# Optimization experiments

Hardware: AMD Instinct MI355X
Metric: run time of the kernel (lower is better)

The kernel has to match this reference:

```python
import jax, jax.numpy as jnp
import numpy as np

B, H, S, D = 2, 16, 2048, 64

def setup_inputs() -> dict:
    key = jax.random.key(0)
    kq, kk, kv = jax.random.split(key, 3)
    q = jax.random.normal(kq, (B, H, S, D), dtype=jnp.float32)
    k = jax.random.normal(kk, (B, H, S, D), dtype=jnp.float32)
    v = jax.random.normal(kv, (B, H, S, D), dtype=jnp.float32)
    mask = jnp.tril(jnp.ones((S, S), dtype=bool))  # causal, broadcast over B,H
    return {"q": q, "k": k, "v": v, "mask": mask}

def reference(q, k, v, mask):
    d_k = q.shape[-1]
    # [..., num_q, num_kv]
    qk = jnp.einsum('bhqd,bhkd->bhqk', q, k) / jnp.sqrt(jnp.asarray(d_k, q.dtype))
    qk = jnp.where(mask, qk, -jnp.inf)
    attn = jax.nn.softmax(qk, axis=-1)
    return jnp.einsum('bhqk,bhkd->bhqd', attn, v)
```

## Files before the change

### kernel.cpp

```cpp
#include <hip/hip_runtime.h>

#define SS 2048
#define DD 64
#define BH 32
#define QSCALE 0.1803368801f
#define NCHUNK 40
#define NSLOT (BH * NCHUNK)
#define BUFS 8448

typedef __attribute__((ext_vector_type(8))) short short8;
typedef __attribute__((ext_vector_type(4))) float floatx4;

__device__ __forceinline__ short f2bf(float x) {
  union { float f; unsigned u; } un; un.f = x;
  unsigned r = (un.u + 0x7FFFu + ((un.u >> 16) & 1u)) >> 16;
  return (short)r;
}
__device__ __forceinline__ short f2bf_fast(float x) {
  union { float f; unsigned u; } un; un.f = x;
  return (short)((un.u + 0x8000u) >> 16);
}
__device__ __forceinline__ float fexp2(float x) {
  return __builtin_amdgcn_exp2f(x);
}
__device__ __forceinline__ void gload16(const short* g, short* l) {
  __builtin_amdgcn_global_load_lds(
      (const __attribute__((address_space(1))) void*)g,
      (__attribute__((address_space(3))) void*)l, 16, 0, 0);
}
#define MFMA __builtin_amdgcn_mfma_f32_16x16x32_bf16

__global__ __launch_bounds__(256) void prep_k(const float* __restrict__ K,
                                              short* __restrict__ Kbf) {
  const size_t i = ((size_t)blockIdx.x * 256 + threadIdx.x) * 8;
  floatx4 a = *(const floatx4*)(K + i);
  floatx4 b = *(const floatx4*)(K + i + 4);
  short8 s;
  s[0]=f2bf(a[0]); s[1]=f2bf(a[1]); s[2]=f2bf(a[2]); s[3]=f2bf(a[3]);
  s[4]=f2bf(b[0]); s[5]=f2bf(b[1]); s[6]=f2bf(b[2]); s[7]=f2bf(b[3]);
  *(short8*)(Kbf + i) = s;
}

__device__ __forceinline__ int kperm(int c) {
  return (((c >> 2) & 1) << 4) + ((c >> 3) << 2) + (c & 3);
}

__global__ __launch_bounds__(256) void prep_vtp(const float* __restrict__ V,
                                                short* __restrict__ Vtp) {
  __shared__ short Ts[64][72];
  const int bh = blockIdx.y;
  const int s0 = blockIdx.x * 64;
  const int t = threadIdx.x;
  {
    const int r = t >> 2, c = (t & 3) * 16;
    const float* g = V + ((size_t)bh * SS + s0 + r) * DD + c;
    floatx4 a = *(const floatx4*)g;
    floatx4 b = *(const floatx4*)(g + 4);
    floatx4 cc = *(const floatx4*)(g + 8);
    floatx4 d = *(const floatx4*)(g + 12);
    short8 x0, x1;
    x0[0]=f2bf(a[0]); x0[1]=f2bf(a[1]); x0[2]=f2bf(a[2]); x0[3]=f2bf(a[3]);
    x0[4]=f2bf(b[0]); x0[5]=f2bf(b[1]); x0[6]=f2bf(b[2]); x0[7]=f2bf(b[3]);
    x1[0]=f2bf(cc[0]);x1[1]=f2bf(cc[1]);x1[2]=f2bf(cc[2]);x1[3]=f2bf(cc[3]);
    x1[4]=f2bf(d[0]); x1[5]=f2bf(d[1]); x1[6]=f2bf(d[2]); x1[7]=f2bf(d[3]);
    *(short8*)&Ts[r][c] = x0;
    *(short8*)&Ts[r][c + 8] = x1;
  }
  __syncthreads();
  {
    const int d = t >> 2, cblk = (t & 3) * 16;
    short8 y0, y1;
    #pragma unroll
    for (int j = 0; j < 8; ++j) {
      const int c0 = cblk + j, c1 = cblk + 8 + j;
      y0[j] = Ts[(c0 & 32) + kperm(c0 & 31)][d];
      y1[j] = Ts[(c1 & 32) + kperm(c1 & 31)][d];
    }
    const int kt  = (s0 + cblk) >> 5;
    const int kin = cblk & 31;
    short* o = Vtp + (((size_t)bh * 64 + kt) * 64 + d) * 32 + kin;
    *(short8*)o = y0;
    *(short8*)(o + 8) = y1;
  }
}

__device__ __forceinline__ void y2qc(int y, int& qt, int& c) {
  if (y < 4)       { qt = y;                            c = 0; }
  else if (y < 12) { int i = y - 4;  qt = 4 + (i >> 1); c = i & 1; }
  else if (y < 24) { int i = y - 12; qt = 8 + i / 3;    c = i - (qt - 8) * 3; }
  else             { int i = y - 24; qt = 12 + (i >> 2); c = i & 3; }
}

__global__ __launch_bounds__(256, 4) void sdpa_part(
    const float* __restrict__ Q, const short* __restrict__ Kbf,
    const short* __restrict__ Vtp, float* __restrict__ PO,
    float* __restrict__ PRS) {
  __shared__ __align__(16) short Sh[2][BUFS];

  const int tid  = threadIdx.x;
  const int w    = tid >> 6;
  const int lane = tid & 63;
  const int quad = lane >> 4;
  const int l16  = lane & 15;

  const int bh = blockIdx.x;
  const int y  = 39 - (int)blockIdx.y;
  int qt, c; y2qc(y, qt, c);
  const int kt0 = c * 16;
  const int kt1 = min(kt0 + 16, 4 * qt + 4);
  const int ktd = 4 * qt + w;
  const int qA  = qt * 128 + w * 32;
  const int qB  = qA + 16;

  const size_t base = (size_t)bh * SS * DD;
  const short* kbase = Kbf + base;
  const short* vtb   = Vtp + (size_t)bh * 64 * 2048;

  {
    const short* gk = kbase + (size_t)kt0 * 2048 + w * 512 + lane * 8;
    gload16(gk,        &Sh[0][w * 544]);
    gload16(gk + 2048, &Sh[0][2176 + w * 544]);
    const short* gv = vtb + (size_t)kt0 * 2048 + w * 512 + lane * 8;
    gload16(gv,        &Sh[0][4352 + w * 512]);
    gload16(gv + 2048, &Sh[0][6400 + w * 512]);
  }

  short8 qaA0, qaA1, qaB0, qaB1;
  {
    const float* ga = Q + base + (size_t)(qA + l16) * DD + quad * 8;
    const float* gb = Q + base + (size_t)(qB + l16) * DD + quad * 8;
    floatx4 a0 = *(const floatx4*)ga,        a1 = *(const floatx4*)(ga + 4);
    floatx4 a2 = *(const floatx4*)(ga + 32), a3 = *(const floatx4*)(ga + 36);
    floatx4 b0 = *(const floatx4*)gb,        b1 = *(const floatx4*)(gb + 4);
    floatx4 b2 = *(const floatx4*)(gb + 32), b3 = *(const floatx4*)(gb + 36);
    #pragma unroll
    for (int j = 0; j < 4; ++j) {
      qaA0[j] = f2bf(a0[j] * QSCALE); qaA0[4 + j] = f2bf(a1[j] * QSCALE);
      qaA1[j] = f2bf(a2[j] * QSCALE); qaA1[4 + j] = f2bf(a3[j] * QSCALE);
      qaB0[j] = f2bf(b0[j] * QSCALE); qaB0[4 + j] = f2bf(b1[j] * QSCALE);
      qaB1[j] = f2bf(b2[j] * QSCALE); qaB1[4 + j] = f2bf(b3[j] * QSCALE);
    }
  }

  short8 ones;
  #pragma unroll
  for (int j = 0; j < 8; ++j) ones[j] = (short)0x3F80;

  floatx4 z = {0.f, 0.f, 0.f, 0.f};
  floatx4 oA0 = z, oA1 = z, oA2 = z, oA3 = z;
  floatx4 oB0 = z, oB1 = z, oB2 = z, oB3 = z;
  floatx4 sA = z, sB = z;

  int nb = 0;
  for (int ktp = kt0; ktp < kt1; ktp += 2) {
    __asm__ volatile("s_waitcnt vmcnt(0)" ::: "memory");
    __syncthreads();

    if (ktp + 2 < kt1) {
      const short* gk = kbase + (size_t)(ktp + 2) * 2048 + w * 512 + lane * 8;
      gload16(gk,        &Sh[nb ^ 1][w * 544]);
      gload16(gk + 2048, &Sh[nb ^ 1][2176 + w * 544]);
      const short* gv = vtb + (size_t)(ktp + 2) * 2048 + w * 512 + lane * 8;
      gload16(gv,        &Sh[nb ^ 1][4352 + w * 512]);
      gload16(gv + 2048, &Sh[nb ^ 1][6400 + w * 512]);
    }

    #pragma unroll
    for (int j = 0; j < 2; ++j) {
      const int kt = ktp + j;
      if (kt <= ktd) {
        const short* lb = &Sh[nb][j * 2176];
        const short* vb = &Sh[nb][4352 + j * 2048];
        const int kro = (l16 >> 3) * 544 + (l16 & 7) * 64 + quad * 8;
        short8 kb00 = *(const short8*)(lb + kro);
        short8 kb01 = *(const short8*)(lb + kro + 32);
        short8 kb10 = *(const short8*)(lb + kro + 1088);
        short8 kb11 = *(const short8*)(lb + kro + 1120);
        const int vro = l16 * 32 + quad * 8;
        short8 vt0 = *(const short8*)(vb + vro);
        short8 vt1 = *(const short8*)(vb + vro + 512);
        short8 vt2 = *(const short8*)(vb + vro + 1024);
        short8 vt3 = *(const short8*)(vb + vro + 1536);

        floatx4 tA0 = z, tA1 = z, tB0 = z, tB1 = z;
        tA0 = MFMA(kb00, qaA0, tA0, 0, 0, 0); tA0 = MFMA(kb01, qaA1, tA0, 0, 0, 0);
        tA1 = MFMA(kb10, qaA0, tA1, 0, 0, 0); tA1 = MFMA(kb11, qaA1, tA1, 0, 0, 0);
        tB0 = MFMA(kb00, qaB0, tB0, 0, 0, 0); tB0 = MFMA(kb01, qaB1, tB0, 0, 0, 0);
        tB1 = MFMA(kb10, qaB0, tB1, 0, 0, 0); tB1 = MFMA(kb11, qaB1, tB1, 0, 0, 0);

        if (kt == ktd) {
          const int kq = quad * 4;
          #pragma unroll
          for (int r = 0; r < 4; ++r) {
            tA0[r] = (kq + r      <= l16)      ? tA0[r] : -1e30f;
            tA1[r] = (kq + r + 16 <= l16)      ? tA1[r] : -1e30f;
            tB0[r] = (kq + r      <= l16 + 16) ? tB0[r] : -1e30f;
            tB1[r] = (kq + r      <= l16)      ? tB1[r] : -1e30f;
          }
        }

        short8 paA, paB;
        #pragma unroll
        for (int r = 0; r < 4; ++r) {
          paA[r]     = f2bf_fast(fexp2(tA0[r]));
          paA[4 + r] = f2bf_fast(fexp2(tA1[r]));
          paB[r]     = f2bf_fast(fexp2(tB0[r]));
          paB[4 + r] = f2bf_fast(fexp2(tB1[r]));
        }

        sA = MFMA(ones, paA, sA, 0, 0, 0);
        sB = MFMA(ones, paB, sB, 0, 0, 0);

        oA0 = MFMA(vt0, paA, oA0, 0, 0, 0); oA1 = MFMA(vt1, paA, oA1, 0, 0, 0);
        oA2 = MFMA(vt2, paA, oA2, 0, 0, 0); oA3 = MFMA(vt3, paA, oA3, 0, 0, 0);
        oB0 = MFMA(vt0, paB, oB0, 0, 0, 0); oB1 = MFMA(vt1, paB, oB1, 0, 0, 0);
        oB2 = MFMA(vt2, paB, oB2, 0, 0, 0); oB3 = MFMA(vt3, paB, oB3, 0, 0, 0);
      }
    }
    nb ^= 1;
  }

  const int slot = bh * NCHUNK + y;
  float* po = PO + (size_t)slot * (128 * 64);
  float* ra = po + (w * 32 + l16) * 64 + quad * 4;
  float* rb = po + (w * 32 + 16 + l16) * 64 + quad * 4;
  *(floatx4*)(ra)      = oA0;
  *(floatx4*)(ra + 16) = oA1;
  *(floatx4*)(ra + 32) = oA2;
  *(floatx4*)(ra + 48) = oA3;
  *(floatx4*)(rb)      = oB0;
  *(floatx4*)(rb + 16) = oB1;
  *(floatx4*)(rb + 32) = oB2;
  *(floatx4*)(rb + 48) = oB3;
  if (quad == 0) {
    PRS[slot * 128 + w * 32 + l16]      = sA[0];
    PRS[slot * 128 + w * 32 + 16 + l16] = sB[0];
  }
}

__global__ __launch_bounds__(256) void sdpa_combine(
    const float* __restrict__ PO, const float* __restrict__ PRS,
    float* __restrict__ O) {
  const int bh  = blockIdx.x;
  const int g32 = blockIdx.y;
  const int qt  = g32 >> 2;
  const int t   = threadIdx.x;
  const int row  = t >> 3;
  const int col  = (t & 7) * 8;
  const int rloc = (g32 & 3) * 32 + row;

  const int g  = qt >> 2;
  const int cn = g + 1;
  int ybase;
  if      (g == 0) ybase = qt;
  else if (g == 1) ybase = 4 + 2 * (qt - 4);
  else if (g == 2) ybase = 12 + 3 * (qt - 8);
  else             ybase = 24 + 4 * (qt - 12);

  floatx4 accL = {0.f,0.f,0.f,0.f}, accH = accL;
  float den = 0.f;
  for (int c = 0; c < cn; ++c) {
    const int slot = bh * NCHUNK + ybase + c;
    const float* po = PO + (size_t)slot * (128 * 64) + rloc * 64 + col;
    floatx4 a = *(const floatx4*)po;
    floatx4 b = *(const floatx4*)(po + 4);
    accL += a; accH += b;
    den += PRS[slot * 128 + rloc];
  }
  const float inv = 1.0f / den;
  accL *= inv; accH *= inv;
  float* out = O + ((size_t)bh * SS + qt * 128 + rloc) * DD + col;
  *(floatx4*)out = accL;
  *(floatx4*)(out + 4) = accH;
}

extern "C" void kernel_launch(void* const* d_in, const int* in_sizes, int n_in,
                              void* d_out, int out_size, void* d_ws, size_t ws_size,
                              hipStream_t stream) {
  (void)in_sizes; (void)n_in; (void)out_size; (void)ws_size;
  const float* q = (const float*)d_in[0];
  const float* k = (const float*)d_in[1];
  const float* v = (const float*)d_in[2];
  float* o = (float*)d_out;

  short* Kbf = (short*)d_ws;
  short* Vtp = Kbf + (size_t)BH * SS * DD;
  float* PO  = (float*)(Vtp + (size_t)BH * SS * DD);
  float* PRS = PO + (size_t)NSLOT * 128 * 64;

  prep_k<<<dim3(BH * SS * DD / 8 / 256), 256, 0, stream>>>(k, Kbf);
  prep_vtp<<<dim3(SS / 64, BH), 256, 0, stream>>>(v, Vtp);
  sdpa_part<<<dim3(BH, NCHUNK), 256, 0, stream>>>(q, Kbf, Vtp, PO, PRS);
  sdpa_combine<<<dim3(BH, SS / 32), 256, 0, stream>>>(PO, PRS, o);
}
```

Baseline: 138.2 us.

## Drop split-KV partials and combine kernel; fuse K/V prep into one kernel

Replaces the 40-chunk split-KV scheme, which wrote partial outputs and row sums and then reduced them in a separate combine kernel, with one block per 128-row query tile that walks every causal key tile and normalises in registers before writing the output. The K bf16 conversion is merged into the V transpose kernel, so the launch count drops from four to two and the partial-buffer round trip to memory goes away. In exchange the grid shrinks to 512 blocks with very uneven per-block work (1 to 16 key-tile pairs). Heavy and light tiles are interleaved in launch order to soften the imbalance, but the longest tile now sets the critical path.

```diff
diff --git a/kernel.cpp b/kernel.cpp
--- a/kernel.cpp
+++ b/kernel.cpp
@@ -4,8 +4,6 @@
 #define DD 64
 #define BH 32
 #define QSCALE 0.1803368801f
-#define NCHUNK 40
-#define NSLOT (BH * NCHUNK)
 #define BUFS 8448
 
 typedef __attribute__((ext_vector_type(8))) short short8;
@@ -30,41 +28,46 @@
 }
 #define MFMA __builtin_amdgcn_mfma_f32_16x16x32_bf16
 
-__global__ __launch_bounds__(256) void prep_k(const float* __restrict__ K,
-                                              short* __restrict__ Kbf) {
-  const size_t i = ((size_t)blockIdx.x * 256 + threadIdx.x) * 8;
-  floatx4 a = *(const floatx4*)(K + i);
-  floatx4 b = *(const floatx4*)(K + i + 4);
-  short8 s;
-  s[0]=f2bf(a[0]); s[1]=f2bf(a[1]); s[2]=f2bf(a[2]); s[3]=f2bf(a[3]);
-  s[4]=f2bf(b[0]); s[5]=f2bf(b[1]); s[6]=f2bf(b[2]); s[7]=f2bf(b[3]);
-  *(short8*)(Kbf + i) = s;
-}
-
 __device__ __forceinline__ int kperm(int c) {
   return (((c >> 2) & 1) << 4) + ((c >> 3) << 2) + (c & 3);
 }
 
-__global__ __launch_bounds__(256) void prep_vtp(const float* __restrict__ V,
-                                                short* __restrict__ Vtp) {
+__global__ __launch_bounds__(256) void prep_kv(const float* __restrict__ K,
+                                               const float* __restrict__ V,
+                                               short* __restrict__ Kbf,
+                                               short* __restrict__ Vtp) {
   __shared__ short Ts[64][72];
   const int bh = blockIdx.y;
-  const int s0 = blockIdx.x * 64;
-  const int t = threadIdx.x;
+  const int r0 = blockIdx.x * 64;
+  const int t  = threadIdx.x;
   {
     const int r = t >> 2, c = (t & 3) * 16;
-    const float* g = V + ((size_t)bh * SS + s0 + r) * DD + c;
+    const float* g = V + ((size_t)bh * SS + r0 + r) * DD + c;
     floatx4 a = *(const floatx4*)g;
     floatx4 b = *(const floatx4*)(g + 4);
     floatx4 cc = *(const floatx4*)(g + 8);
-    floatx4 d = *(const floatx4*)(g + 12);
+    floatx4 dd = *(const floatx4*)(g + 12);
     short8 x0, x1;
     x0[0]=f2bf(a[0]); x0[1]=f2bf(a[1]); x0[2]=f2bf(a[2]); x0[3]=f2bf(a[3]);
     x0[4]=f2bf(b[0]); x0[5]=f2bf(b[1]); x0[6]=f2bf(b[2]); x0[7]=f2bf(b[3]);
     x1[0]=f2bf(cc[0]);x1[1]=f2bf(cc[1]);x1[2]=f2bf(cc[2]);x1[3]=f2bf(cc[3]);
-    x1[4]=f2bf(d[0]); x1[5]=f2bf(d[1]); x1[6]=f2bf(d[2]); x1[7]=f2bf(d[3]);
+    x1[4]=f2bf(dd[0]);x1[5]=f2bf(dd[1]);x1[6]=f2bf(dd[2]);x1[7]=f2bf(dd[3]);
     *(short8*)&Ts[r][c] = x0;
     *(short8*)&Ts[r][c + 8] = x1;
+  }
+  {
+    const size_t i = ((size_t)bh * SS + r0) * DD + (size_t)t * 16;
+    floatx4 a = *(const floatx4*)(K + i);
+    floatx4 b = *(const floatx4*)(K + i + 4);
+    floatx4 cc = *(const floatx4*)(K + i + 8);
+    floatx4 dd = *(const floatx4*)(K + i + 12);
+    short8 x0, x1;
+    x0[0]=f2bf(a[0]); x0[1]=f2bf(a[1]); x0[2]=f2bf(a[2]); x0[3]=f2bf(a[3]);
+    x0[4]=f2bf(b[0]); x0[5]=f2bf(b[1]); x0[6]=f2bf(b[2]); x0[7]=f2bf(b[3]);
+    x1[0]=f2bf(cc[0]);x1[1]=f2bf(cc[1]);x1[2]=f2bf(cc[2]);x1[3]=f2bf(cc[3]);
+    x1[4]=f2bf(dd[0]);x1[5]=f2bf(dd[1]);x1[6]=f2bf(dd[2]);x1[7]=f2bf(dd[3]);
+    *(short8*)(Kbf + i) = x0;
+    *(short8*)(Kbf + i + 8) = x1;
   }
   __syncthreads();
   {
@@ -76,7 +79,7 @@
       y0[j] = Ts[(c0 & 32) + kperm(c0 & 31)][d];
       y1[j] = Ts[(c1 & 32) + kperm(c1 & 31)][d];
     }
-    const int kt  = (s0 + cblk) >> 5;
+    const int kt  = (r0 + cblk) >> 5;
     const int kin = cblk & 31;
     short* o = Vtp + (((size_t)bh * 64 + kt) * 64 + d) * 32 + kin;
     *(short8*)o = y0;
@@ -84,17 +87,9 @@
   }
 }
 
-__device__ __forceinline__ void y2qc(int y, int& qt, int& c) {
-  if (y < 4)       { qt = y;                            c = 0; }
-  else if (y < 12) { int i = y - 4;  qt = 4 + (i >> 1); c = i & 1; }
-  else if (y < 24) { int i = y - 12; qt = 8 + i / 3;    c = i - (qt - 8) * 3; }
-  else             { int i = y - 24; qt = 12 + (i >> 2); c = i & 3; }
-}
-
-__global__ __launch_bounds__(256, 4) void sdpa_part(
+__global__ __launch_bounds__(256, 4) void sdpa_fused(
     const float* __restrict__ Q, const short* __restrict__ Kbf,
-    const short* __restrict__ Vtp, float* __restrict__ PO,
-    float* __restrict__ PRS) {
+    const short* __restrict__ Vtp, float* __restrict__ Og) {
   __shared__ __align__(16) short Sh[2][BUFS];
 
   const int tid  = threadIdx.x;
@@ -104,23 +99,22 @@
   const int l16  = lane & 15;
 
   const int bh = blockIdx.x;
-  const int y  = 39 - (int)blockIdx.y;
-  int qt, c; y2qc(y, qt, c);
-  const int kt0 = c * 16;
-  const int kt1 = min(kt0 + 16, 4 * qt + 4);
+  const int y  = blockIdx.y;
+  const int qt = (y < 8) ? (15 - y) : (y - 8);
+  const int ktn = 4 * qt + 4;
   const int ktd = 4 * qt + w;
   const int qA  = qt * 128 + w * 32;
   const int qB  = qA + 16;
 
   const size_t base = (size_t)bh * SS * DD;
   const short* kbase = Kbf + base;
-  const short* vtb   = Vtp + (size_t)bh * 64 * 2048;
-
-  {
-    const short* gk = kbase + (size_t)kt0 * 2048 + w * 512 + lane * 8;
+  const short* vtb   = Vtp + base;
+
+  {
+    const short* gk = kbase + w * 512 + lane * 8;
     gload16(gk,        &Sh[0][w * 544]);
     gload16(gk + 2048, &Sh[0][2176 + w * 544]);
-    const short* gv = vtb + (size_t)kt0 * 2048 + w * 512 + lane * 8;
+    const short* gv = vtb + w * 512 + lane * 8;
     gload16(gv,        &Sh[0][4352 + w * 512]);
     gload16(gv + 2048, &Sh[0][6400 + w * 512]);
   }
@@ -152,11 +146,11 @@
   floatx4 sA = z, sB = z;
 
   int nb = 0;
-  for (int ktp = kt0; ktp < kt1; ktp += 2) {
+  for (int ktp = 0; ktp < ktn; ktp += 2) {
     __asm__ volatile("s_waitcnt vmcnt(0)" ::: "memory");
     __syncthreads();
 
-    if (ktp + 2 < kt1) {
+    if (ktp + 2 < ktn) {
       const short* gk = kbase + (size_t)(ktp + 2) * 2048 + w * 512 + lane * 8;
       gload16(gk,        &Sh[nb ^ 1][w * 544]);
       gload16(gk + 2048, &Sh[nb ^ 1][2176 + w * 544]);
@@ -220,10 +214,13 @@
     nb ^= 1;
   }
 
-  const int slot = bh * NCHUNK + y;
-  float* po = PO + (size_t)slot * (128 * 64);
-  float* ra = po + (w * 32 + l16) * 64 + quad * 4;
-  float* rb = po + (w * 32 + 16 + l16) * 64 + quad * 4;
+  const float invA = 1.0f / sA[0];
+  const float invB = 1.0f / sB[0];
+  oA0 *= invA; oA1 *= invA; oA2 *= invA; oA3 *= invA;
+  oB0 *= invB; oB1 *= invB; oB2 *= invB; oB3 *= invB;
+
+  float* ra = Og + base + (size_t)(qA + l16) * DD + quad * 4;
+  float* rb = Og + base + (size_t)(qB + l16) * DD + quad * 4;
   *(floatx4*)(ra)      = oA0;
   *(floatx4*)(ra + 16) = oA1;
   *(floatx4*)(ra + 32) = oA2;
@@ -232,46 +229,6 @@
   *(floatx4*)(rb + 16) = oB1;
   *(floatx4*)(rb + 32) = oB2;
   *(floatx4*)(rb + 48) = oB3;
-  if (quad == 0) {
-    PRS[slot * 128 + w * 32 + l16]      = sA[0];
-    PRS[slot * 128 + w * 32 + 16 + l16] = sB[0];
-  }
-}
-
-__global__ __launch_bounds__(256) void sdpa_combine(
-    const float* __restrict__ PO, const float* __restrict__ PRS,
-    float* __restrict__ O) {
-  const int bh  = blockIdx.x;
-  const int g32 = blockIdx.y;
-  const int qt  = g32 >> 2;
-  const int t   = threadIdx.x;
-  const int row  = t >> 3;
-  const int col  = (t & 7) * 8;
-  const int rloc = (g32 & 3) * 32 + row;
-
-  const int g  = qt >> 2;
-  const int cn = g + 1;
-  int ybase;
-  if      (g == 0) ybase = qt;
-  else if (g == 1) ybase = 4 + 2 * (qt - 4);
-  else if (g == 2) ybase = 12 + 3 * (qt - 8);
-  else             ybase = 24 + 4 * (qt - 12);
-
-  floatx4 accL = {0.f,0.f,0.f,0.f}, accH = accL;
-  float den = 0.f;
-  for (int c = 0; c < cn; ++c) {
-    const int slot = bh * NCHUNK + ybase + c;
-    const float* po = PO + (size_t)slot * (128 * 64) + rloc * 64 + col;
-    floatx4 a = *(const floatx4*)po;
-    floatx4 b = *(const floatx4*)(po + 4);
-    accL += a; accH += b;
-    den += PRS[slot * 128 + rloc];
-  }
-  const float inv = 1.0f / den;
-  accL *= inv; accH *= inv;
-  float* out = O + ((size_t)bh * SS + qt * 128 + rloc) * DD + col;
-  *(floatx4*)out = accL;
-  *(floatx4*)(out + 4) = accH;
 }
 
 extern "C" void kernel_launch(void* const* d_in, const int* in_sizes, int n_in,
@@ -285,11 +242,7 @@
 
   short* Kbf = (short*)d_ws;
   short* Vtp = Kbf + (size_t)BH * SS * DD;
-  float* PO  = (float*)(Vtp + (size_t)BH * SS * DD);
-  float* PRS = PO + (size_t)NSLOT * 128 * 64;
-
-  prep_k<<<dim3(BH * SS * DD / 8 / 256), 256, 0, stream>>>(k, Kbf);
-  prep_vtp<<<dim3(SS / 64, BH), 256, 0, stream>>>(v, Vtp);
-  sdpa_part<<<dim3(BH, NCHUNK), 256, 0, stream>>>(q, Kbf, Vtp, PO, PRS);
-  sdpa_combine<<<dim3(BH, SS / 32), 256, 0, stream>>>(PO, PRS, o);
-}
+
+  prep_kv<<<dim3(SS / 64, BH), 256, 0, stream>>>(k, v, Kbf, Vtp);
+  sdpa_fused<<<dim3(BH, 16), 256, 0, stream>>>(q, Kbf, Vtp, o);
+}
```

Result: faster. 131.6 us (-4.8%).
